# Optimization experiments

Measured on AMD Instinct MI355X. Metric: run time of the kernel, lower is better.

The kernel has to match this reference:

```python
import jax, jax.numpy as jnp
import numpy as np

B, N, C, NH, AG, HW = 16, 3136, 256, 8, 49, 56

def setup_inputs() -> dict:
    key = jax.random.key(0)
    ks = jax.random.split(key, 14)
    f = lambda k, shp, s=0.02: jax.random.normal(k, shp, jnp.float32) * s
    return {
        "x_f": jax.random.normal(ks[0], (B, N, C), jnp.float32),
        "x_t": jax.random.normal(ks[1], (B, N, C), jnp.float32),
        "Wq": f(ks[2], (C, C)),
        "Wkv": f(ks[3], (C, 2 * C)),
        "Wproj": f(ks[4], (C, C)),
        "bproj": jnp.zeros((C,), jnp.float32),
        "dwc_w": f(ks[5], (C, 1, 3, 3), 0.1),   # depthwise 3x3, groups=C (OIHW, I=1)
        "dwc_b": jnp.zeros((C,), jnp.float32),
        "an_bias": f(ks[6], (NH, AG, 7, 7)),
        "na_bias": f(ks[7], (NH, AG, 7, 7)),
        "ah_bias": f(ks[8], (1, NH, AG, HW, 1)),
        "aw_bias": f(ks[9], (1, NH, AG, 1, HW)),
        "ha_bias": f(ks[10], (1, NH, HW, 1, AG)),
        "wa_bias": f(ks[11], (1, NH, 1, HW, AG)),
        "H": HW,
        "W": HW,
    }

def reference(x_f, x_t, Wq, Wkv, Wproj, bproj, dwc_w, dwc_b,
              an_bias, na_bias, ah_bias, aw_bias, ha_bias, wa_bias, H, W):
    b, n, c = x_f.shape
    h, ag = an_bias.shape[0], an_bias.shape[1]
    d = c // h
    scale = d ** (-0.5)
    ps = int(ag ** 0.5)  # agent grid side (7)

    q = x_f @ Wq                       # [b,n,c]
    kv = x_t @ Wkv                     # [b,n,2c]
    k, v = kv[..., :c], kv[..., c:]

    # agent tokens: adaptive avg-pool q over (H,W) -> (ps,ps); H%ps==0 so exact 8x8 block means
    agent = q.reshape(b, ps, H // ps, ps, W // ps, c).mean(axis=(2, 4)).reshape(b, ag, c)

    heads = lambda t, L: t.reshape(b, L, h, d).transpose(0, 2, 1, 3)
    qh, kh, vh, ah = heads(q, n), heads(k, n), heads(v, n), heads(agent, ag)

    # stage 1: agent <- kv attention, bias = bilinear(an_bias 7x7 -> HxW) + (ah + aw)
    pb1 = jax.image.resize(an_bias, (h, ag, H, W), method='bilinear').reshape(1, h, ag, n)
    pb2 = (ah_bias + aw_bias).reshape(1, h, ag, n)
    agent_attn = jax.nn.softmax(scale * jnp.einsum('bhad,bhnd->bhan', ah, kh) + pb1 + pb2, axis=-1)
    agent_v = jnp.einsum('bhan,bhnd->bhad', agent_attn, vh)  # [b,h,ag,d]

    # stage 2: query <- agent attention, bias = bilinear(na_bias)^T + (ha + wa)
    ab1 = jax.image.resize(na_bias, (h, ag, H, W), method='bilinear').reshape(1, h, ag, n).transpose(0, 1, 3, 2)
    ab2 = (ha_bias + wa_bias).reshape(1, h, n, ag)
    q_attn = jax.nn.softmax(scale * jnp.einsum('bhnd,bhad->bhna', qh, ah) + ab1 + ab2, axis=-1)
    x = jnp.einsum('bhna,bhad->bhnd', q_attn, agent_v).transpose(0, 2, 1, 3).reshape(b, n, c)

    # depthwise-conv residual on v
    v_img = vh.transpose(0, 2, 1, 3).reshape(b, H, W, c).transpose(0, 3, 1, 2)  # [b,c,H,W]
    dwc = jax.lax.conv_general_dilated(v_img, dwc_w, (1, 1), 'SAME',
                                       feature_group_count=c,
                                       dimension_numbers=('NCHW', 'OIHW', 'NCHW'))
    dwc = dwc + dwc_b[None, :, None, None]
    x = x + dwc.transpose(0, 2, 3, 1).reshape(b, n, c)

    return x @ Wproj + bproj
```

## Files before the change

### kernel.cpp

```cpp
#include <hip/hip_runtime.h>
#include <hip/hip_bf16.h>

namespace {
constexpr int kB  = 16;
constexpr int kN  = 3136;
constexpr int kC  = 256;
constexpr int kH  = 8;
constexpr int kD  = 32;
constexpr int kAG = 49;
constexpr int kHW = 56;
constexpr int kKV = 512;
constexpr int kSEG = 7;
constexpr int kPART = 33;

constexpr int BM = 128, BN = 128, BK = 64;
constexpr int LDK = BK + 8;

constexpr int kNT = kN / 256 + 1;
}

typedef __attribute__((ext_vector_type(8))) short short8;
typedef __attribute__((ext_vector_type(8))) unsigned short ushort8;
typedef __attribute__((ext_vector_type(4))) unsigned short ushort4v;
typedef __attribute__((ext_vector_type(4))) float f32x4;

__device__ __forceinline__ unsigned short f2bf(float f) {
  union { float f; unsigned u; } v; v.f = f;
  unsigned r = (v.u + 0x7FFF + ((v.u >> 16) & 1)) >> 16;
  return (unsigned short)r;
}
__device__ __forceinline__ float bf2f(unsigned short u) {
  union { unsigned u; float f; } v; v.u = ((unsigned)u) << 16;
  return v.f;
}

__device__ __forceinline__ float bilin7(const float* __restrict__ tab, int y, int x) {
  float fy = (y + 0.5f) * 0.125f - 0.5f;
  float fx = (x + 0.5f) * 0.125f - 0.5f;
  float fy0 = floorf(fy), fx0 = floorf(fx);
  float wy = fy - fy0, wx = fx - fx0;
  int y0 = (int)fy0, x0 = (int)fx0;
  int y0c = min(6, max(0, y0)),     x0c = min(6, max(0, x0));
  int y1c = min(6, max(0, y0 + 1)), x1c = min(6, max(0, x0 + 1));
  float v00 = tab[y0c * 7 + x0c], v01 = tab[y0c * 7 + x1c];
  float v10 = tab[y1c * 7 + x0c], v11 = tab[y1c * 7 + x1c];
  float top = v00 + wx * (v01 - v00);
  float bot = v10 + wx * (v11 - v10);
  return top + wy * (bot - top);
}

__global__ __launch_bounds__(256) void wtrans_kernel(
    const float* __restrict__ W, unsigned short* __restrict__ Wt, int K, int N) {
  int idx = blockIdx.x * 256 + threadIdx.x;
  if (idx >= K * N) return;
  int n = idx / K, k = idx - n * K;
  Wt[idx] = f2bf(W[(size_t)k * N + n]);
}

template <bool ABF16, bool OUTBF16>
__global__ __launch_bounds__(256) void gemm_mixed_kernel(
    const void* __restrict__ Ap, const unsigned short* __restrict__ Bt,
    const float* __restrict__ bias, void* __restrict__ Cp,
    int M, int Nn, int K) {
  __shared__ unsigned short As[BM * LDK];
  __shared__ unsigned short Bs[BN * LDK];
  const int t = threadIdx.x;

  int tx = blockIdx.x, ty = blockIdx.y;
  {
    int nwg = gridDim.x * gridDim.y;
    if ((nwg & 7) == 0) {
      int bid = ty * gridDim.x + tx;
      int per8 = nwg >> 3;
      int lt = (bid & 7) * per8 + (bid >> 3);
      tx = lt % gridDim.x;
      ty = lt / gridDim.x;
    }
  }
  const int row0 = ty * BM;
  const int col0 = tx * BN;
  const int lane = t & 63;
  const int wid  = t >> 6;
  const int wrow = (wid >> 1) * 64;
  const int wcol = (wid & 1) * 64;
  const int lr = lane & 15, lg = lane >> 4;

  f32x4 acc[4][4] = {};

  for (int k0 = 0; k0 < K; k0 += BK) {
    __syncthreads();
    if constexpr (ABF16) {
      const unsigned short* A = (const unsigned short*)Ap;
#pragma unroll
      for (int i = 0; i < 4; ++i) {
        int idx = t + i * 256;
        int r = idx >> 3, k8 = (idx & 7) * 8;
        *(ushort8*)&As[r * LDK + k8] =
            *(const ushort8*)&A[(size_t)(row0 + r) * K + k0 + k8];
      }
    } else {
      const float* A = (const float*)Ap;
#pragma unroll
      for (int i = 0; i < 8; ++i) {
        int idx = t + i * 256;
        int r = idx >> 4, k4 = (idx & 15) * 4;
        float4 f = *(const float4*)&A[(size_t)(row0 + r) * K + k0 + k4];
        unsigned lo = (unsigned)f2bf(f.x) | ((unsigned)f2bf(f.y) << 16);
        unsigned hi = (unsigned)f2bf(f.z) | ((unsigned)f2bf(f.w) << 16);
        *(uint2*)&As[r * LDK + k4] = make_uint2(lo, hi);
      }
    }
#pragma unroll
    for (int i = 0; i < 4; ++i) {
      int idx = t + i * 256;
      int r = idx >> 3, k8 = (idx & 7) * 8;
      *(ushort8*)&Bs[r * LDK + k8] =
          *(const ushort8*)&Bt[(size_t)(col0 + r) * K + k0 + k8];
    }
    __syncthreads();
#pragma unroll
    for (int ks = 0; ks < 2; ++ks) {
      short8 af[4], bf[4];
#pragma unroll
      for (int m = 0; m < 4; ++m)
        af[m] = *(const short8*)&As[(wrow + m * 16 + lr) * LDK + ks * 32 + lg * 8];
#pragma unroll
      for (int n = 0; n < 4; ++n)
        bf[n] = *(const short8*)&Bs[(wcol + n * 16 + lr) * LDK + ks * 32 + lg * 8];
#pragma unroll
      for (int m = 0; m < 4; ++m)
#pragma unroll
        for (int n = 0; n < 4; ++n)
          acc[m][n] = __builtin_amdgcn_mfma_f32_16x16x32_bf16(
              af[m], bf[n], acc[m][n], 0, 0, 0);
    }
  }
#pragma unroll
  for (int m = 0; m < 4; ++m) {
#pragma unroll
    for (int n = 0; n < 4; ++n) {
      int col = col0 + wcol + n * 16 + lr;
      float badd = bias ? bias[col] : 0.f;
#pragma unroll
      for (int j = 0; j < 4; ++j) {
        int row = row0 + wrow + m * 16 + lg * 4 + j;
        if constexpr (OUTBF16)
          ((unsigned short*)Cp)[(size_t)row * Nn + col] = f2bf(acc[m][n][j] + badd);
        else
          ((float*)Cp)[(size_t)row * Nn + col] = acc[m][n][j] + badd;
      }
    }
  }
}

__global__ __launch_bounds__(256) void pool_kernel(const unsigned short* __restrict__ q,
                                                   float* __restrict__ agent) {
  int blk = blockIdx.x;
  int b = blk / kAG, a = blk % kAG;
  int ho = a / 7, wo = a % 7;
  int c = threadIdx.x;
  float s = 0.f;
#pragma unroll
  for (int i = 0; i < 8; ++i) {
    int y = ho * 8 + i;
#pragma unroll
    for (int j = 0; j < 8; ++j) {
      int x = wo * 8 + j;
      s += bf2f(q[((size_t)b * kN + y * kHW + x) * kC + c]);
    }
  }
  agent[((size_t)b * kAG + a) * kC + c] = s * (1.f / 64.f);
}

__global__ __launch_bounds__(256) void abias_kernel(
    const float* __restrict__ an_bias, const float* __restrict__ ah_bias,
    const float* __restrict__ aw_bias, float* __restrict__ abias) {
  int ha = blockIdx.x;
  const float* tab = an_bias + ha * 49;
  const float* ahb = ah_bias + ha * kHW;
  const float* awb = aw_bias + ha * kHW;
  for (int n = threadIdx.x; n < kN; n += 256) {
    int y = n / kHW, x = n % kHW;
    abias[(size_t)ha * kN + n] = bilin7(tab, y, x) + ahb[y] + awb[x];
  }
}

__global__ __launch_bounds__(256) void agent_attn_flash3_kernel(
    const float* __restrict__ agent, const unsigned short* __restrict__ kv,
    const float* __restrict__ abias, float* __restrict__ part) {
  const int t = threadIdx.x;
  const int lin = blockIdx.x;
  const int h = lin & 7;
  const int r = lin >> 3;
  const int seg = r % kSEG;
  const int b = r / kSEG;
  const int w = t >> 6, lane = t & 63;
  const int lr = lane & 15, lg = lane >> 4;
  const float scale = 0.17677669529663687f;

  __shared__ char sh[36864];
  unsigned short* agsT = (unsigned short*)sh;
  unsigned short* Pa   = (unsigned short*)(sh + 5120) + w * 64 * 40;
  unsigned short* Vt   = (unsigned short*)(sh + 25600) + w * 32 * 40;
  float* lred = (float*)(sh + 35840);

  for (int i = t; i < 320; i += 256) *(ushort8*)&agsT[i * 8] = (ushort8)0;
  __syncthreads();
  for (int i = t; i < kAG * 4; i += 256) {
    int a = i >> 2, j = i & 3;
    const float* sp = agent + ((size_t)b * kAG + a) * kC + h * kD + j * 8;
    float4 f0 = *(const float4*)sp, f1 = *(const float4*)(sp + 4);
    ushort8 v;
    v[0] = f2bf(f0.x); v[1] = f2bf(f0.y); v[2] = f2bf(f0.z); v[3] = f2bf(f0.w);
    v[4] = f2bf(f1.x); v[5] = f2bf(f1.y); v[6] = f2bf(f1.z); v[7] = f2bf(f1.w);
    *(ushort8*)&agsT[a * 40 + j * 8] = v;
  }
  __syncthreads();

  float ls[4] = {};
  f32x4 o[4][2] = {};
  const int nchunks = (w < 2) ? 4 : 3;
  for (int ci = 0; ci < nchunks; ++ci) {
    const int chunk = w + 4 * ci;
    const int nb0 = seg * 448 + chunk * 32;
    {
      int n = lane & 31, d0 = (lane >> 5) * 16;
      const unsigned short* vp =
          kv + ((size_t)b * kN + nb0 + n) * kKV + kC + h * kD + d0;
      ushort8 v0 = *(const ushort8*)vp;
      ushort8 v1 = *(const ushort8*)(vp + 8);
#pragma unroll
      for (int e = 0; e < 8; ++e) Vt[(d0 + e) * 40 + n] = v0[e];
#pragma unroll
      for (int e = 0; e < 8; ++e) Vt[(d0 + 8 + e) * 40 + n] = v1[e];
    }
    short8 af0 = *(const short8*)&kv[((size_t)b * kN + nb0 + lr) * kKV + h * kD + lg * 8];
    short8 af1 = *(const short8*)&kv[((size_t)b * kN + nb0 + 16 + lr) * kKV + h * kD + lg * 8];
    f32x4 c[2][4] = {};
#pragma unroll
    for (int ct = 0; ct < 4; ++ct) {
      short8 bfr = *(const short8*)&agsT[(ct * 16 + lr) * 40 + lg * 8];
      c[0][ct] = __builtin_amdgcn_mfma_f32_16x16x32_bf16(af0, bfr, c[0][ct], 0, 0, 0);
      c[1][ct] = __builtin_amdgcn_mfma_f32_16x16x32_bf16(af1, bfr, c[1][ct], 0, 0, 0);
    }
#pragma unroll
    for (int rt = 0; rt < 2; ++rt) {
#pragma unroll
      for (int ct = 0; ct < 4; ++ct) {
        int a = ct * 16 + lr;
        bool valid = a < kAG;
        float4 ab = {0.f, 0.f, 0.f, 0.f};
        if (valid)
          ab = *(const float4*)&abias[((size_t)(h * kAG + a)) * kN + nb0 + rt * 16 + lg * 4];
        unsigned lo, hi;
        {
          float p0 = valid ? __expf(fmaf(c[rt][ct][0], scale, ab.x)) : 0.f;
          float p1 = valid ? __expf(fmaf(c[rt][ct][1], scale, ab.y)) : 0.f;
          float p2 = valid ? __expf(fmaf(c[rt][ct][2], scale, ab.z)) : 0.f;
          float p3 = valid ? __expf(fmaf(c[rt][ct][3], scale, ab.w)) : 0.f;
          ls[ct] += (p0 + p1) + (p2 + p3);
          lo = (unsigned)f2bf(p0) | ((unsigned)f2bf(p1) << 16);
          hi = (unsigned)f2bf(p2) | ((unsigned)f2bf(p3) << 16);
        }
        *(uint2*)&Pa[a * 40 + rt * 16 + lg * 4] = make_uint2(lo, hi);
      }
    }
    short8 bfv0 = *(const short8*)&Vt[(lr) * 40 + lg * 8];
    short8 bfv1 = *(const short8*)&Vt[(16 + lr) * 40 + lg * 8];
#pragma unroll
    for (int rt = 0; rt < 4; ++rt) {
      short8 afp = *(const short8*)&Pa[(rt * 16 + lr) * 40 + lg * 8];
      o[rt][0] = __builtin_amdgcn_mfma_f32_16x16x32_bf16(afp, bfv0, o[rt][0], 0, 0, 0);
      o[rt][1] = __builtin_amdgcn_mfma_f32_16x16x32_bf16(afp, bfv1, o[rt][1], 0, 0, 0);
    }
  }
#pragma unroll
  for (int ct = 0; ct < 4; ++ct) {
    ls[ct] += __shfl_xor(ls[ct], 16);
    ls[ct] += __shfl_xor(ls[ct], 32);
  }
  __syncthreads();
  float* ored = (float*)sh;
  if (lane < 16) {
#pragma unroll
    for (int ct = 0; ct < 4; ++ct) lred[w * 64 + ct * 16 + lane] = ls[ct];
  }
#pragma unroll
  for (int rt = 0; rt < 4; ++rt)
#pragma unroll
    for (int ct2 = 0; ct2 < 2; ++ct2)
#pragma unroll
      for (int reg = 0; reg < 4; ++reg)
        ored[(w * 64 + rt * 16 + lg * 4 + reg) * 33 + ct2 * 16 + lr] =
            o[rt][ct2][reg];
  __syncthreads();
  float* pb = part + (((size_t)(b * kH + h)) * kSEG + seg) * (kAG * kPART);
  if (t < kAG)
    pb[t * kPART] = lred[t] + lred[64 + t] + lred[128 + t] + lred[192 + t];
  for (int i = t; i < kAG * kD; i += 256) {
    int a = i >> 5, d = i & 31;
    float s = ored[a * 33 + d] + ored[(64 + a) * 33 + d]
            + ored[(128 + a) * 33 + d] + ored[(192 + a) * 33 + d];
    pb[a * kPART + 1 + d] = s;
  }
}

__global__ __launch_bounds__(256) void agent_merge_kernel(
    const float* __restrict__ part, float* __restrict__ agent_v) {
  int g = blockIdx.x * 256 + threadIdx.x;
  int d = g & 31;
  int a = (g >> 5) % kAG;
  int bh = g / (kAG * kD);
  const float* pb = part + (((size_t)bh) * kSEG) * (kAG * kPART) + a * kPART;
  float den = 0.f, num = 0.f;
#pragma unroll
  for (int s = 0; s < kSEG; ++s) {
    const float* p = pb + s * kAG * kPART;
    den += p[0];
    num += p[1 + d];
  }
  agent_v[g] = num / den;
}

__global__ __launch_bounds__(256) void qbias_kernel(
    const float* __restrict__ na_bias, const float* __restrict__ ha_bias,
    const float* __restrict__ wa_bias, unsigned short* __restrict__ qbias) {
  int ha = blockIdx.x;
  int h = ha / kAG, a = ha % kAG;
  const float* tab = na_bias + ha * 49;
  for (int n = threadIdx.x; n < kN; n += 256) {
    int y = n / kHW, x = n % kHW;
    qbias[(size_t)ha * kN + n] = f2bf(bilin7(tab, y, x)
        + ha_bias[(h * kHW + y) * kAG + a]
        + wa_bias[(h * kHW + x) * kAG + a]);
  }
}

__global__ __launch_bounds__(256) void qattn_v9_kernel(
    unsigned short* __restrict__ q, const unsigned short* __restrict__ kv,
    const float* __restrict__ agent, const float* __restrict__ agent_v,
    const unsigned short* __restrict__ qbias, const float* __restrict__ dwc_w,
    const float* __restrict__ dwc_b) {
  const int t = threadIdx.x;
  int lin = blockIdx.x + gridDim.x * (blockIdx.y + gridDim.y * blockIdx.z);
  const int h = lin & 7;
  int rest = lin >> 3;
  const int n0 = (rest % kNT) * 256;
  const int b  = rest / kNT;
  const int w = t >> 6, lane = t & 63;
  const int lr = lane & 15, lg = lane >> 4;
  const float scale = 0.17677669529663687f;

  __shared__ unsigned short agsT[64 * 40];
  __shared__ unsigned short avsT[32 * 72];
  __shared__ unsigned short PW[4][2560];

  for (int i = t; i < 320; i += 256) *(ushort8*)&agsT[i * 8] = (ushort8)0;
  for (int i = t; i < 288; i += 256) *(ushort8*)&avsT[i * 8] = (ushort8)0;
  __syncthreads();
  for (int i = t; i < kAG * 4; i += 256) {
    int a = i >> 2, j = i & 3;
    const float* sp = agent + ((size_t)b * kAG + a) * kC + h * kD + j * 8;
    float4 f0 = *(const float4*)sp, f1 = *(const float4*)(sp + 4);
    ushort8 v;
    v[0] = f2bf(f0.x); v[1] = f2bf(f0.y); v[2] = f2bf(f0.z); v[3] = f2bf(f0.w);
    v[4] = f2bf(f1.x); v[5] = f2bf(f1.y); v[6] = f2bf(f1.z); v[7] = f2bf(f1.w);
    *(ushort8*)&agsT[a * 40 + j * 8] = v;
  }
  for (int i = t; i < kAG * 8; i += 256) {
    int a = i >> 3, dj = i & 7;
    float4 f = *(const float4*)(agent_v + (((size_t)b * kH + h) * kAG + a) * kD + dj * 4);
    avsT[(dj * 4 + 0) * 72 + a] = f2bf(f.x);
    avsT[(dj * 4 + 1) * 72 + a] = f2bf(f.y);
    avsT[(dj * 4 + 2) * 72 + a] = f2bf(f.z);
    avsT[(dj * 4 + 3) * 72 + a] = f2bf(f.w);
  }
  __syncthreads();

  short8 af[4];
#pragma unroll
  for (int rt = 0; rt < 4; ++rt) {
    int nr = n0 + w * 64 + rt * 16 + lr;
    nr = min(nr, kN - 1);
    af[rt] = *(const short8*)&q[((size_t)b * kN + nr) * kC + h * kD + lg * 8];
  }
  short8 bfr[4];
#pragma unroll
  for (int ct = 0; ct < 4; ++ct)
    bfr[ct] = *(const short8*)&agsT[(ct * 16 + lr) * 40 + lg * 8];
  f32x4 c[4][4] = {};
#pragma unroll
  for (int rt = 0; rt < 4; ++rt)
#pragma unroll
    for (int ct = 0; ct < 4; ++ct)
      c[rt][ct] = __builtin_amdgcn_mfma_f32_16x16x32_bf16(af[rt], bfr[ct],
                                                          c[rt][ct], 0, 0, 0);
  f32x4 lsumv[4] = {};
#pragma unroll
  for (int rt = 0; rt < 4; ++rt) {
#pragma unroll
    for (int ct = 0; ct < 4; ++ct) {
      int col = ct * 16 + lr;
      bool valid = col < kAG;
      int nrow = n0 + w * 64 + rt * 16 + lg * 4;
      nrow = min(nrow, kN - 4);
      float qb[4] = {0.f, 0.f, 0.f, 0.f};
      if (valid) {
        uint2 qw = *(const uint2*)&qbias[((size_t)(h * kAG + col)) * kN + nrow];
        qb[0] = bf2f((unsigned short)(qw.x & 0xffff));
        qb[1] = bf2f((unsigned short)(qw.x >> 16));
        qb[2] = bf2f((unsigned short)(qw.y & 0xffff));
        qb[3] = bf2f((unsigned short)(qw.y >> 16));
      }
#pragma unroll
      for (int reg = 0; reg < 4; ++reg) {
        float pv = valid ? __expf(fmaf(c[rt][ct][reg], scale, qb[reg])) : 0.f;
        c[rt][ct][reg] = pv;
        lsumv[rt][reg] += pv;
      }
    }
  }
#pragma unroll
  for (int rt = 0; rt < 4; ++rt)
#pragma unroll
    for (int j = 0; j < 4; ++j) {
      float v = lsumv[rt][j];
      v += __shfl_xor(v, 1);
      v += __shfl_xor(v, 2);
      v += __shfl_xor(v, 4);
      v += __shfl_xor(v, 8);
      lsumv[rt][j] = v;
    }
  unsigned short* Pw = PW[w];
  short8 bf2v[2][2];
#pragma unroll
  for (int ct2 = 0; ct2 < 2; ++ct2)
#pragma unroll
    for (int ks = 0; ks < 2; ++ks)
      bf2v[ct2][ks] = *(const short8*)&avsT[(ct2 * 16 + lr) * 72 + ks * 32 + lg * 8];
  f32x4 o[4][2] = {};
#pragma unroll
  for (int half = 0; half < 2; ++half) {
#pragma unroll
    for (int rt2 = 0; rt2 < 2; ++rt2)
#pragma unroll
      for (int ct = 0; ct < 4; ++ct)
#pragma unroll
        for (int reg = 0; reg < 4; ++reg)
          Pw[(rt2 * 16 + lg * 4 + reg) * 72 + ct * 16 + lr] =
              f2bf(c[half * 2 + rt2][ct][reg]);
#pragma unroll
    for (int rt2 = 0; rt2 < 2; ++rt2) {
      short8 afp[2];
#pragma unroll
      for (int ks = 0; ks < 2; ++ks)
        afp[ks] = *(const short8*)&Pw[(rt2 * 16 + lr) * 72 + ks * 32 + lg * 8];
      int rt = half * 2 + rt2;
#pragma unroll
      for (int ct2 = 0; ct2 < 2; ++ct2)
#pragma unroll
        for (int ks = 0; ks < 2; ++ks)
          o[rt][ct2] = __builtin_amdgcn_mfma_f32_16x16x32_bf16(
              afp[ks], bf2v[ct2][ks], o[rt][ct2], 0, 0, 0);
    }
  }
#pragma unroll
  for (int rt = 0; rt < 4; ++rt) {
    f32x4 inv;
#pragma unroll
    for (int j = 0; j < 4; ++j) inv[j] = 1.f / lsumv[rt][j];
#pragma unroll
    for (int ct2 = 0; ct2 < 2; ++ct2)
#pragma unroll
      for (int reg = 0; reg < 4; ++reg)
        Pw[(rt * 16 + lg * 4 + reg) * 36 + ct2 * 16 + lr] =
            f2bf(o[rt][ct2][reg] * inv[reg]);
  }
  const int n = n0 + t;
  if (n >= kN) return;
  const unsigned short* orow = &PW[w][(t & 63) * 36];
  float out[kD];
#pragma unroll
  for (int d4 = 0; d4 < 8; ++d4) {
    ushort4v v = *(const ushort4v*)&orow[d4 * 4];
#pragma unroll
    for (int e = 0; e < 4; ++e) out[d4 * 4 + e] = bf2f(v[e]);
  }
  const float* wb = dwc_w + (h * kD) * 9;
  const float* bb = dwc_b + h * kD;
#pragma unroll
  for (int d = 0; d < kD; ++d) out[d] += bb[d];
  const int y = n / kHW, x = n % kHW;
#pragma unroll
  for (int ky = 0; ky < 3; ++ky) {
    int yy = y + ky - 1;
    if (yy < 0 || yy >= kHW) continue;
#pragma unroll
    for (int kx = 0; kx < 3; ++kx) {
      int xx = x + kx - 1;
      if (xx < 0 || xx >= kHW) continue;
      const unsigned short* vp =
          kv + ((size_t)b * kN + yy * kHW + xx) * kKV + kC + h * kD;
#pragma unroll
      for (int d8 = 0; d8 < 4; ++d8) {
        ushort8 vv = *(const ushort8*)(vp + d8 * 8);
#pragma unroll
        for (int e = 0; e < 8; ++e)
          out[d8 * 8 + e] = fmaf(wb[(d8 * 8 + e) * 9 + ky * 3 + kx],
                                 bf2f(vv[e]), out[d8 * 8 + e]);
      }
    }
  }
  unsigned short* qp = q + ((size_t)b * kN + n) * kC + h * kD;
#pragma unroll
  for (int d8 = 0; d8 < 4; ++d8) {
    ushort8 v;
#pragma unroll
    for (int e = 0; e < 8; ++e) v[e] = f2bf(out[d8 * 8 + e]);
    *(ushort8*)(qp + d8 * 8) = v;
  }
}

extern "C" void kernel_launch(void* const* d_in, const int* in_sizes, int n_in,
                              void* d_out, int out_size, void* d_ws, size_t ws_size,
                              hipStream_t stream) {
  const float* x_f     = (const float*)d_in[0];
  const float* x_t     = (const float*)d_in[1];
  const float* Wq      = (const float*)d_in[2];
  const float* Wkv     = (const float*)d_in[3];
  const float* Wproj   = (const float*)d_in[4];
  const float* bproj   = (const float*)d_in[5];
  const float* dwc_w   = (const float*)d_in[6];
  const float* dwc_b   = (const float*)d_in[7];
  const float* an_bias = (const float*)d_in[8];
  const float* na_bias = (const float*)d_in[9];
  const float* ah_bias = (const float*)d_in[10];
  const float* aw_bias = (const float*)d_in[11];
  const float* ha_bias = (const float*)d_in[12];
  const float* wa_bias = (const float*)d_in[13];
  float* out           = (float*)d_out;

  const size_t qbiasN = (size_t)kH * kAG * kN;
  const size_t perbB = (size_t)kN * kC * 2 + (size_t)kN * kKV * 2
                     + ((size_t)kAG * kC + (size_t)kH * kAG * kD
                        + (size_t)kH * kSEG * kAG * kPART) * 4;
  const size_t wtE = (size_t)kC * kC + (size_t)kC * kKV + (size_t)kC * kC;
  const size_t tabB = qbiasN * 2 + qbiasN * 4 + wtE * 2;
  if (ws_size < tabB) return;
  size_t fit = (ws_size - tabB) / perbB;
  int chunk = (int)(fit < 16 ? fit : 16);
  if (chunk < 1) return;

  char* p = (char*)d_ws;
  unsigned short* qbias = (unsigned short*)p;  p += qbiasN * 2;
  float* abias = (float*)p;                    p += qbiasN * 4;
  unsigned short* WqT   = (unsigned short*)p;  p += (size_t)kC * kC * 2;
  unsigned short* WkvT  = (unsigned short*)p;  p += (size_t)kC * kKV * 2;
  unsigned short* WprojT= (unsigned short*)p;  p += (size_t)kC * kC * 2;
  unsigned short* q  = (unsigned short*)p;     p += (size_t)chunk * kN * kC * 2;
  unsigned short* kv = (unsigned short*)p;     p += (size_t)chunk * kN * kKV * 2;
  float* agent  = (float*)p;                   p += (size_t)chunk * kAG * kC * 4;
  float* agentv = (float*)p;                   p += (size_t)chunk * kH * kAG * kD * 4;
  float* part   = (float*)p;

  qbias_kernel<<<kH * kAG, 256, 0, stream>>>(na_bias, ha_bias, wa_bias, qbias);
  abias_kernel<<<kH * kAG, 256, 0, stream>>>(an_bias, ah_bias, aw_bias, abias);
  wtrans_kernel<<<(kC * kC + 255) / 256, 256, 0, stream>>>(Wq, WqT, kC, kC);
  wtrans_kernel<<<(kC * kKV + 255) / 256, 256, 0, stream>>>(Wkv, WkvT, kC, kKV);
  wtrans_kernel<<<(kC * kC + 255) / 256, 256, 0, stream>>>(Wproj, WprojT, kC, kC);

  for (int b0 = 0; b0 < kB; b0 += chunk) {
    int nb = (kB - b0) < chunk ? (kB - b0) : chunk;
    const int M = nb * kN;
    const float* xf_c = x_f + (size_t)b0 * kN * kC;
    const float* xt_c = x_t + (size_t)b0 * kN * kC;
    float* out_c = out + (size_t)b0 * kN * kC;

    gemm_mixed_kernel<false, true><<<dim3(kC / BN, M / BM), 256, 0, stream>>>(
        xf_c, WqT, nullptr, q, M, kC, kC);
    gemm_mixed_kernel<false, true><<<dim3(kKV / BN, M / BM), 256, 0, stream>>>(
        xt_c, WkvT, nullptr, kv, M, kKV, kC);
    pool_kernel<<<nb * kAG, 256, 0, stream>>>(q, agent);
    agent_attn_flash3_kernel<<<nb * kH * kSEG, 256, 0, stream>>>(agent, kv, abias, part);
    agent_merge_kernel<<<nb * kAG, 256, 0, stream>>>(part, agentv);
    qattn_v9_kernel<<<dim3(kNT, kH, nb), 256, 0, stream>>>(
        q, kv, agent, agentv, qbias, dwc_w, dwc_b);
    gemm_mixed_kernel<true, false><<<dim3(kC / BN, M / BM), 256, 0, stream>>>(
        q, WprojT, bproj, out_c, M, kC, kC);
  }
}
```

Measured before the change: 219.9 us.

## Store q/k/v head-major and reuse output buffer for k/v scratch

The projection GEMMs now write q, k and v in a head-major [b,h,n,d] bf16 layout so the attention, pooling and depthwise-conv kernels read contiguous per-head rows instead of strided 512-wide rows. When workspace is large enough, all 16 batches run in a single pass. In that path the k/v intermediates are stored in the output buffer, which the final projection then overwrites. This is meant to improve coalescing and cut launch count, but the GEMM epilogues now use scattered 2-byte stores with per-element divisions, and the final GEMM's A loads become gathered across heads.

```diff
diff --git a/kernel.cpp b/kernel.cpp
--- a/kernel.cpp
+++ b/kernel.cpp
@@ -57,10 +57,10 @@
   Wt[idx] = f2bf(W[(size_t)k * N + n]);
 }
 
-template <bool ABF16, bool OUTBF16>
+template <int AMODE, int OMODE>
 __global__ __launch_bounds__(256) void gemm_mixed_kernel(
     const void* __restrict__ Ap, const unsigned short* __restrict__ Bt,
-    const float* __restrict__ bias, void* __restrict__ Cp,
+    const float* __restrict__ bias, void* __restrict__ Cp, void* __restrict__ Cp2,
     int M, int Nn, int K) {
   __shared__ unsigned short As[BM * LDK];
   __shared__ unsigned short Bs[BN * LDK];
@@ -89,14 +89,17 @@
 
   for (int k0 = 0; k0 < K; k0 += BK) {
     __syncthreads();
-    if constexpr (ABF16) {
+    if constexpr (AMODE == 1) {
       const unsigned short* A = (const unsigned short*)Ap;
 #pragma unroll
       for (int i = 0; i < 4; ++i) {
         int idx = t + i * 256;
         int r = idx >> 3, k8 = (idx & 7) * 8;
-        *(ushort8*)&As[r * LDK + k8] =
-            *(const ushort8*)&A[(size_t)(row0 + r) * K + k0 + k8];
+        int row = row0 + r;
+        int bb = row / kN, nn = row - bb * kN;
+        int k = k0 + k8;
+        *(ushort8*)&As[r * LDK + k8] = *(const ushort8*)&A[
+            (((size_t)bb * kH + (k >> 5)) * kN + nn) * kD + (k & 31)];
       }
     } else {
       const float* A = (const float*)Ap;
@@ -140,25 +143,43 @@
 #pragma unroll
     for (int n = 0; n < 4; ++n) {
       int col = col0 + wcol + n * 16 + lr;
-      float badd = bias ? bias[col] : 0.f;
+      float badd = 0.f;
+      if constexpr (OMODE == 0) badd = bias ? bias[col] : 0.f;
 #pragma unroll
       for (int j = 0; j < 4; ++j) {
         int row = row0 + wrow + m * 16 + lg * 4 + j;
-        if constexpr (OUTBF16)
-          ((unsigned short*)Cp)[(size_t)row * Nn + col] = f2bf(acc[m][n][j] + badd);
-        else
+        if constexpr (OMODE == 0) {
           ((float*)Cp)[(size_t)row * Nn + col] = acc[m][n][j] + badd;
+        } else {
+          int bb = row / kN, nn = row - bb * kN;
+          unsigned short val = f2bf(acc[m][n][j]);
+          if constexpr (OMODE == 1) {
+            ((unsigned short*)Cp)[(((size_t)bb * kH + (col >> 5)) * kN + nn) * kD
+                                  + (col & 31)] = val;
+          } else {
+            if (col < kC)
+              ((unsigned short*)Cp)[(((size_t)bb * kH + (col >> 5)) * kN + nn) * kD
+                                    + (col & 31)] = val;
+            else {
+              int c2 = col - kC;
+              ((unsigned short*)Cp2)[(((size_t)bb * kH + (c2 >> 5)) * kN + nn) * kD
+                                     + (c2 & 31)] = val;
+            }
+          }
+        }
       }
     }
   }
 }
 
-__global__ __launch_bounds__(256) void pool_kernel(const unsigned short* __restrict__ q,
+__global__ __launch_bounds__(256) void pool_kernel(const unsigned short* __restrict__ qT,
                                                    float* __restrict__ agent) {
   int blk = blockIdx.x;
   int b = blk / kAG, a = blk % kAG;
   int ho = a / 7, wo = a % 7;
   int c = threadIdx.x;
+  int h = c >> 5, d = c & 31;
+  const unsigned short* base = qT + ((size_t)b * kH + h) * kN * kD + d;
   float s = 0.f;
 #pragma unroll
   for (int i = 0; i < 8; ++i) {
@@ -166,7 +187,7 @@
 #pragma unroll
     for (int j = 0; j < 8; ++j) {
       int x = wo * 8 + j;
-      s += bf2f(q[((size_t)b * kN + y * kHW + x) * kC + c]);
+      s += bf2f(base[(size_t)(y * kHW + x) * kD]);
     }
   }
   agent[((size_t)b * kAG + a) * kC + c] = s * (1.f / 64.f);
@@ -185,9 +206,10 @@
   }
 }
 
-__global__ __launch_bounds__(256) void agent_attn_flash3_kernel(
-    const float* __restrict__ agent, const unsigned short* __restrict__ kv,
-    const float* __restrict__ abias, float* __restrict__ part) {
+__global__ __launch_bounds__(256) void agent_attn_flash4_kernel(
+    const float* __restrict__ agent, const unsigned short* __restrict__ kT,
+    const unsigned short* __restrict__ vT, const float* __restrict__ abias,
+    float* __restrict__ part) {
   const int t = threadIdx.x;
   const int lin = blockIdx.x;
   const int h = lin & 7;
@@ -203,6 +225,9 @@
   unsigned short* Pa   = (unsigned short*)(sh + 5120) + w * 64 * 40;
   unsigned short* Vt   = (unsigned short*)(sh + 25600) + w * 32 * 40;
   float* lred = (float*)(sh + 35840);
+
+  const unsigned short* kH_ = kT + ((size_t)b * kH + h) * kN * kD;
+  const unsigned short* vH_ = vT + ((size_t)b * kH + h) * kN * kD;
 
   for (int i = t; i < 320; i += 256) *(ushort8*)&agsT[i * 8] = (ushort8)0;
   __syncthreads();
@@ -225,8 +250,7 @@
     const int nb0 = seg * 448 + chunk * 32;
     {
       int n = lane & 31, d0 = (lane >> 5) * 16;
-      const unsigned short* vp =
-          kv + ((size_t)b * kN + nb0 + n) * kKV + kC + h * kD + d0;
+      const unsigned short* vp = vH_ + (size_t)(nb0 + n) * kD + d0;
       ushort8 v0 = *(const ushort8*)vp;
       ushort8 v1 = *(const ushort8*)(vp + 8);
 #pragma unroll
@@ -234,8 +258,8 @@
 #pragma unroll
       for (int e = 0; e < 8; ++e) Vt[(d0 + 8 + e) * 40 + n] = v1[e];
     }
-    short8 af0 = *(const short8*)&kv[((size_t)b * kN + nb0 + lr) * kKV + h * kD + lg * 8];
-    short8 af1 = *(const short8*)&kv[((size_t)b * kN + nb0 + 16 + lr) * kKV + h * kD + lg * 8];
+    short8 af0 = *(const short8*)&kH_[(size_t)(nb0 + lr) * kD + lg * 8];
+    short8 af1 = *(const short8*)&kH_[(size_t)(nb0 + 16 + lr) * kD + lg * 8];
     f32x4 c[2][4] = {};
 #pragma unroll
     for (int ct = 0; ct < 4; ++ct) {
@@ -336,8 +360,8 @@
   }
 }
 
-__global__ __launch_bounds__(256) void qattn_v9_kernel(
-    unsigned short* __restrict__ q, const unsigned short* __restrict__ kv,
+__global__ __launch_bounds__(256) void qattn_v10_kernel(
+    unsigned short* __restrict__ qT, const unsigned short* __restrict__ vT,
     const float* __restrict__ agent, const float* __restrict__ agent_v,
     const unsigned short* __restrict__ qbias, const float* __restrict__ dwc_w,
     const float* __restrict__ dwc_b) {
@@ -351,6 +375,9 @@
   const int lr = lane & 15, lg = lane >> 4;
   const float scale = 0.17677669529663687f;
 
+  unsigned short* qH_ = qT + ((size_t)b * kH + h) * kN * kD;
+  const unsigned short* vH_ = vT + ((size_t)b * kH + h) * kN * kD;
+
   __shared__ unsigned short agsT[64 * 40];
   __shared__ unsigned short avsT[32 * 72];
   __shared__ unsigned short PW[4][2560];
@@ -382,7 +409,7 @@
   for (int rt = 0; rt < 4; ++rt) {
     int nr = n0 + w * 64 + rt * 16 + lr;
     nr = min(nr, kN - 1);
-    af[rt] = *(const short8*)&q[((size_t)b * kN + nr) * kC + h * kD + lg * 8];
+    af[rt] = *(const short8*)&qH_[(size_t)nr * kD + lg * 8];
   }
   short8 bfr[4];
 #pragma unroll
@@ -499,8 +526,7 @@
     for (int kx = 0; kx < 3; ++kx) {
       int xx = x + kx - 1;
       if (xx < 0 || xx >= kHW) continue;
-      const unsigned short* vp =
-          kv + ((size_t)b * kN + yy * kHW + xx) * kKV + kC + h * kD;
+      const unsigned short* vp = vH_ + (size_t)(yy * kHW + xx) * kD;
 #pragma unroll
       for (int d8 = 0; d8 < 4; ++d8) {
         ushort8 vv = *(const ushort8*)(vp + d8 * 8);
@@ -511,7 +537,7 @@
       }
     }
   }
-  unsigned short* qp = q + ((size_t)b * kN + n) * kC + h * kD;
+  unsigned short* qp = qH_ + (size_t)n * kD;
 #pragma unroll
   for (int d8 = 0; d8 < 4; ++d8) {
     ushort8 v;
@@ -541,15 +567,16 @@
   float* out           = (float*)d_out;
 
   const size_t qbiasN = (size_t)kH * kAG * kN;
-  const size_t perbB = (size_t)kN * kC * 2 + (size_t)kN * kKV * 2
-                     + ((size_t)kAG * kC + (size_t)kH * kAG * kD
-                        + (size_t)kH * kSEG * kAG * kPART) * 4;
   const size_t wtE = (size_t)kC * kC + (size_t)kC * kKV + (size_t)kC * kC;
   const size_t tabB = qbiasN * 2 + qbiasN * 4 + wtE * 2;
   if (ws_size < tabB) return;
-  size_t fit = (ws_size - tabB) / perbB;
-  int chunk = (int)(fit < 16 ? fit : 16);
-  if (chunk < 1) return;
+
+  const size_t headE = (size_t)kB * kH * kN * kD;
+  const size_t qFullB   = headE * 2;
+  const size_t agentB   = (size_t)kB * kAG * kC * 4;
+  const size_t agentvB  = (size_t)kB * kH * kAG * kD * 4;
+  const size_t partB    = (size_t)kB * kH * kSEG * kAG * kPART * 4;
+  const size_t fullWsB  = tabB + qFullB + agentB + agentvB + partB;
 
   char* p = (char*)d_ws;
   unsigned short* qbias = (unsigned short*)p;  p += qbiasN * 2;
@@ -557,17 +584,51 @@
   unsigned short* WqT   = (unsigned short*)p;  p += (size_t)kC * kC * 2;
   unsigned short* WkvT  = (unsigned short*)p;  p += (size_t)kC * kKV * 2;
   unsigned short* WprojT= (unsigned short*)p;  p += (size_t)kC * kC * 2;
-  unsigned short* q  = (unsigned short*)p;     p += (size_t)chunk * kN * kC * 2;
-  unsigned short* kv = (unsigned short*)p;     p += (size_t)chunk * kN * kKV * 2;
-  float* agent  = (float*)p;                   p += (size_t)chunk * kAG * kC * 4;
-  float* agentv = (float*)p;                   p += (size_t)chunk * kH * kAG * kD * 4;
-  float* part   = (float*)p;
 
   qbias_kernel<<<kH * kAG, 256, 0, stream>>>(na_bias, ha_bias, wa_bias, qbias);
   abias_kernel<<<kH * kAG, 256, 0, stream>>>(an_bias, ah_bias, aw_bias, abias);
   wtrans_kernel<<<(kC * kC + 255) / 256, 256, 0, stream>>>(Wq, WqT, kC, kC);
   wtrans_kernel<<<(kC * kKV + 255) / 256, 256, 0, stream>>>(Wkv, WkvT, kC, kKV);
   wtrans_kernel<<<(kC * kC + 255) / 256, 256, 0, stream>>>(Wproj, WprojT, kC, kC);
+
+  if (ws_size >= fullWsB) {
+    unsigned short* qT = (unsigned short*)p;   p += qFullB;
+    float* agent  = (float*)p;                 p += agentB;
+    float* agentv = (float*)p;                 p += agentvB;
+    float* part   = (float*)p;
+    unsigned short* kT = (unsigned short*)d_out;
+    unsigned short* vT = kT + headE;
+
+    const int M = kB * kN;
+    gemm_mixed_kernel<0, 1><<<dim3(kC / BN, M / BM), 256, 0, stream>>>(
+        x_f, WqT, nullptr, qT, nullptr, M, kC, kC);
+    gemm_mixed_kernel<0, 2><<<dim3(kKV / BN, M / BM), 256, 0, stream>>>(
+        x_t, WkvT, nullptr, kT, vT, M, kKV, kC);
+    pool_kernel<<<kB * kAG, 256, 0, stream>>>(qT, agent);
+    agent_attn_flash4_kernel<<<kB * kH * kSEG, 256, 0, stream>>>(agent, kT, vT,
+                                                                 abias, part);
+    agent_merge_kernel<<<kB * kAG, 256, 0, stream>>>(part, agentv);
+    qattn_v10_kernel<<<dim3(kNT, kH, kB), 256, 0, stream>>>(
+        qT, vT, agent, agentv, qbias, dwc_w, dwc_b);
+    gemm_mixed_kernel<1, 0><<<dim3(kC / BN, M / BM), 256, 0, stream>>>(
+        qT, WprojT, bproj, out, nullptr, M, kC, kC);
+    return;
+  }
+
+  const size_t perbB = (size_t)kH * kN * kD * 2 * 3
+                     + ((size_t)kAG * kC + (size_t)kH * kAG * kD
+                        + (size_t)kH * kSEG * kAG * kPART) * 4;
+  size_t fit = (ws_size - tabB) / perbB;
+  int chunk = (int)(fit < 16 ? fit : 16);
+  if (chunk < 1) return;
+
+  const size_t headEc = (size_t)chunk * kH * kN * kD;
+  unsigned short* qT = (unsigned short*)p;     p += headEc * 2;
+  unsigned short* kT = (unsigned short*)p;     p += headEc * 2;
+  unsigned short* vT = (unsigned short*)p;     p += headEc * 2;
+  float* agent  = (float*)p;                   p += (size_t)chunk * kAG * kC * 4;
+  float* agentv = (float*)p;                   p += (size_t)chunk * kH * kAG * kD * 4;
+  float* part   = (float*)p;
 
   for (int b0 = 0; b0 < kB; b0 += chunk) {
     int nb = (kB - b0) < chunk ? (kB - b0) : chunk;
@@ -576,16 +637,17 @@
     const float* xt_c = x_t + (size_t)b0 * kN * kC;
     float* out_c = out + (size_t)b0 * kN * kC;
 
-    gemm_mixed_kernel<false, true><<<dim3(kC / BN, M / BM), 256, 0, stream>>>(
-        xf_c, WqT, nullptr, q, M, kC, kC);
-    gemm_mixed_kernel<false, true><<<dim3(kKV / BN, M / BM), 256, 0, stream>>>(
-        xt_c, WkvT, nullptr, kv, M, kKV, kC);
-    pool_kernel<<<nb * kAG, 256, 0, stream>>>(q, agent);
-    agent_attn_flash3_kernel<<<nb * kH * kSEG, 256, 0, stream>>>(agent, kv, abias, part);
+    gemm_mixed_kernel<0, 1><<<dim3(kC / BN, M / BM), 256, 0, stream>>>(
+        xf_c, WqT, nullptr, qT, nullptr, M, kC, kC);
+    gemm_mixed_kernel<0, 2><<<dim3(kKV / BN, M / BM), 256, 0, stream>>>(
+        xt_c, WkvT, nullptr, kT, vT, M, kKV, kC);
+    pool_kernel<<<nb * kAG, 256, 0, stream>>>(qT, agent);
+    agent_attn_flash4_kernel<<<nb * kH * kSEG, 256, 0, stream>>>(agent, kT, vT,
+                                                                 abias, part);
     agent_merge_kernel<<<nb * kAG, 256, 0, stream>>>(part, agentv);
-    qattn_v9_kernel<<<dim3(kNT, kH, nb), 256, 0, stream>>>(
-        q, kv, agent, agentv, qbias, dwc_w, dwc_b);
-    gemm_mixed_kernel<true, false><<<dim3(kC / BN, M / BM), 256, 0, stream>>>(
-        q, WprojT, bproj, out_c, M, kC, kC);
-  }
-}
+    qattn_v10_kernel<<<dim3(kNT, kH, nb), 256, 0, stream>>>(
+        qT, vT, agent, agentv, qbias, dwc_w, dwc_b);
+    gemm_mixed_kernel<1, 0><<<dim3(kC / BN, M / BM), 256, 0, stream>>>(
+        qT, WprojT, bproj, out_c, nullptr, M, kC, kC);
+  }
+}
```

Result: faster. 190.7 us, median of 2 (-13.3%).
